# Optimization experiments

Measured on AMD Instinct MI355X. Metric: run time of the kernel, lower is better.

The kernel has to match this reference:

```python
import jax, jax.numpy as jnp
import numpy as np

NUM_ENTS = 100000
NUM_RELS2 = 1000  # num_rels * 2
H_DIM = 128
NUM_EDGES = 2000000
RRELU_SLOPE = (1.0 / 8.0 + 1.0 / 3.0) / 2.0  # F.rrelu eval-mode negative slope


def l2_normalize(x, eps=1e-12):
    # F.normalize along last dim
    n = jnp.sqrt(jnp.sum(x * x, axis=-1, keepdims=True))
    return x / jnp.maximum(n, eps)


def setup_inputs() -> dict:
    key = jax.random.key(0)
    ks = jax.random.split(key, 11)
    s = 1.0 / np.sqrt(H_DIM)
    return {
        "ent_emb": jax.random.normal(ks[0], (NUM_ENTS, H_DIM), jnp.float32),
        "rel_emb": jax.random.normal(ks[1], (NUM_RELS2, H_DIM), jnp.float32) * s,
        "his": jax.random.normal(ks[2], (NUM_ENTS, H_DIM), jnp.float32),
        "W_neighbor": jax.random.normal(ks[3], (H_DIM, H_DIM), jnp.float32) * s,
        "W_self": jax.random.normal(ks[4], (H_DIM, H_DIM), jnp.float32) * s,
        "time_gate_weight": jax.random.normal(ks[5], (H_DIM, H_DIM), jnp.float32) * s,
        "time_gate_bias": jnp.zeros((H_DIM,), jnp.float32),
        "edge_norm": jax.random.uniform(ks[6], (NUM_EDGES,), jnp.float32),
        "src": jax.random.randint(ks[7], (NUM_EDGES,), 0, NUM_ENTS, jnp.int32),
        "dst": jax.random.randint(ks[8], (NUM_EDGES,), 0, NUM_ENTS, jnp.int32),
        "etype": jax.random.randint(ks[9], (NUM_EDGES,), 0, NUM_RELS2, jnp.int32),
    }


def reference(ent_emb, rel_emb, his, W_neighbor, W_self, time_gate_weight,
              time_gate_bias, edge_norm, src, dst, etype):
    # layer_norm=True branch: L2-normalize entity embeddings (F.normalize)
    h = l2_normalize(ent_emb)                                   # [N, D]
    # UnionRGCNLayer message: (h[src] + rel_emb[etype]) @ W, scaled by edge norm
    node = h[src] + rel_emb[etype]                              # [E, D] gather
    msg = (node @ W_neighbor) * edge_norm[:, None]              # [E, D]
    agg = jax.ops.segment_sum(msg, dst, num_segments=NUM_ENTS)  # [N, D] scatter
    # self-loop + rrelu (eval mode: leaky with mean slope)
    h_cur = agg + h @ W_self
    h_cur = jnp.where(h_cur >= 0, h_cur, RRELU_SLOPE * h_cur)
    # time gate: blend current with historical embedding
    gate = jax.nn.sigmoid(h_cur @ time_gate_weight + time_gate_bias)
    out = gate * h_cur + (1.0 - gate) * his
    return out
```

## Files before the change

### kernel.cpp

```cpp
#include <hip/hip_runtime.h>
#include <math.h>

#define NUM_ENTS   100000
#define HD         128
#define NUM_EDGES  2000000
#define NUM_RELS2  1000
#define RRELU_SLOPE 0.22916666666666666f
#define NBLK 391
#define NPAD (NBLK * 256)

#define SB_CNT 391
#define SB_HB  25000
#define SB_RB  125
#define SB_WP  24
#define SB_TOTAL (SB_CNT + SB_HB + SB_RB + SB_WP)

typedef __attribute__((ext_vector_type(8))) short bf16x8;
typedef __attribute__((ext_vector_type(4))) float f32x4;

__device__ __forceinline__ float bf2f(unsigned short h) {
    union { unsigned int u; float f; } v;
    v.u = ((unsigned int)h) << 16;
    return v.f;
}
__device__ __forceinline__ void unpack2(unsigned int u, float& lo, float& hi) {
    union { unsigned int u; float f; } a, b;
    a.u = u << 16;
    b.u = u & 0xffff0000u;
    lo = a.f; hi = b.f;
}
__device__ __forceinline__ unsigned short f2bf(float f) {
    union { float f; unsigned int u; } v; v.f = f;
    unsigned int r = 0x7fffu + ((v.u >> 16) & 1u);
    return (unsigned short)((v.u + r) >> 16);
}

__global__ void __launch_bounds__(256)
setup_kernel(const float* __restrict__ ent, const float* __restrict__ rel,
             const float* __restrict__ Wn, const float* __restrict__ Ws,
             const float* __restrict__ Wt,
             int* __restrict__ cnt, unsigned short* __restrict__ hb,
             unsigned short* __restrict__ rb, unsigned short* __restrict__ Wp) {
    const int bid = blockIdx.x, tid = threadIdx.x;
    if (bid < SB_CNT) {
        cnt[bid * 256 + tid] = 0;
    } else if (bid < SB_CNT + SB_HB) {
        const int row = (bid - SB_CNT) * 4 + (tid >> 6);
        const int lane = tid & 63;
        const float2 v = *(const float2*)(ent + (size_t)row * HD + lane * 2);
        float ss = v.x * v.x + v.y * v.y;
        #pragma unroll
        for (int m = 1; m < 64; m <<= 1) ss += __shfl_xor(ss, m, 64);
        const float inv = 1.0f / fmaxf(sqrtf(ss), 1e-12f);
        const unsigned int o = (unsigned int)f2bf(v.x * inv) |
                               ((unsigned int)f2bf(v.y * inv) << 16);
        *(unsigned int*)(hb + (size_t)row * HD + lane * 2) = o;
    } else if (bid < SB_CNT + SB_HB + SB_RB) {
        const int i = (bid - SB_CNT - SB_HB) * 256 + tid;
        const float4 v = ((const float4*)rel)[i];
        ushort4 o;
        o.x = f2bf(v.x); o.y = f2bf(v.y); o.z = f2bf(v.z); o.w = f2bf(v.w);
        ((ushort4*)rb)[i] = o;
    } else {
        const int blk = (bid - SB_CNT - SB_HB - SB_RB) * 4 + (tid >> 6);
        const int lane = tid & 63;
        const int w = blk >> 5, rem = blk & 31, t = rem >> 2, kt = rem & 3;
        const float* W = (w == 0) ? Wn : (w == 1) ? Ws : Wt;
        const int n  = t * 16 + (lane & 15);
        const int k0 = kt * 32 + (lane >> 4) * 8;
        unsigned short tmp[8];
        #pragma unroll
        for (int j = 0; j < 8; ++j) tmp[j] = f2bf(W[(size_t)(k0 + j) * HD + n]);
        unsigned short* d = Wp + ((size_t)blk * 64 + lane) * 8;
        *(ushort4*)(d + 0) = make_ushort4(tmp[0], tmp[1], tmp[2], tmp[3]);
        *(ushort4*)(d + 4) = make_ushort4(tmp[4], tmp[5], tmp[6], tmp[7]);
    }
}

__global__ void __launch_bounds__(256)
hist_kernel(const int* __restrict__ dst, int* __restrict__ cnt, int* __restrict__ pos) {
    for (int e = blockIdx.x * 256 + threadIdx.x; e < NUM_EDGES; e += gridDim.x * 256)
        pos[e] = atomicAdd(&cnt[dst[e]], 1);
}

__global__ void __launch_bounds__(256)
scan1_kernel(const int* __restrict__ cnt, int* __restrict__ offs, int* __restrict__ bsum) {
    __shared__ int tmp[256];
    const int t = threadIdx.x;
    const int i = blockIdx.x * 256 + t;
    const int v = cnt[i];
    tmp[t] = v;
    __syncthreads();
    #pragma unroll
    for (int d = 1; d < 256; d <<= 1) {
        const int a = (t >= d) ? tmp[t - d] : 0;
        __syncthreads();
        tmp[t] += a;
        __syncthreads();
    }
    offs[i] = tmp[t] - v;
    if (t == 255) bsum[blockIdx.x] = tmp[255];
}

__global__ void __launch_bounds__(512)
scan2_kernel(int* __restrict__ bsum) {
    __shared__ int tmp[512];
    const int t = threadIdx.x;
    const int v = (t < NBLK) ? bsum[t] : 0;
    tmp[t] = v;
    __syncthreads();
    #pragma unroll
    for (int d = 1; d < 512; d <<= 1) {
        const int a = (t >= d) ? tmp[t - d] : 0;
        __syncthreads();
        tmp[t] += a;
        __syncthreads();
    }
    if (t < NBLK) bsum[t] = tmp[t] - v;
}

__global__ void __launch_bounds__(256)
scan3_kernel(int* __restrict__ offs, const int* __restrict__ bsum) {
    const int i = blockIdx.x * 256 + threadIdx.x;
    offs[i] += bsum[blockIdx.x];
}

__global__ void __launch_bounds__(256)
permute_kernel(const int* __restrict__ dst, const int* __restrict__ src,
               const int* __restrict__ ety, const float* __restrict__ enorm,
               const int* __restrict__ offs, const int* __restrict__ pos,
               uint2* __restrict__ recs) {
    for (int e = blockIdx.x * 256 + threadIdx.x; e < NUM_EDGES; e += gridDim.x * 256) {
        const int p = offs[dst[e]] + pos[e];
        uint2 rc;
        rc.x = (unsigned int)src[e] | ((unsigned int)ety[e] << 17);
        rc.y = __float_as_uint(enorm[e]);
        recs[p] = rc;
    }
}

__device__ __forceinline__ void accum8(float* acc, uint4 hv, uint4 rv, float w) {
    float h0, h1, r0, r1;
    unpack2(hv.x, h0, h1); unpack2(rv.x, r0, r1);
    acc[0] += (h0 + r0) * w; acc[1] += (h1 + r1) * w;
    unpack2(hv.y, h0, h1); unpack2(rv.y, r0, r1);
    acc[2] += (h0 + r0) * w; acc[3] += (h1 + r1) * w;
    unpack2(hv.z, h0, h1); unpack2(rv.z, r0, r1);
    acc[4] += (h0 + r0) * w; acc[5] += (h1 + r1) * w;
    unpack2(hv.w, h0, h1); unpack2(rv.w, r0, r1);
    acc[6] += (h0 + r0) * w; acc[7] += (h1 + r1) * w;
}

__global__ void __launch_bounds__(256)
gather_kernel(const unsigned short* __restrict__ hb,
              const unsigned short* __restrict__ rb,
              const int* __restrict__ offs,
              const uint2* __restrict__ recs,
              float* __restrict__ S) {
    const int tid = threadIdx.x;
    const int wv = tid >> 6, lane = tid & 63;
    const int grp = lane >> 4, sub = lane & 15;
    const int d = (blockIdx.x * 4 + wv) * 4 + grp;
    const int beg = offs[d], end = offs[d + 1];
    int i = beg;
    float acc[8] = {0.f, 0.f, 0.f, 0.f, 0.f, 0.f, 0.f, 0.f};
    const unsigned short* hbp = hb + sub * 8;
    const unsigned short* rbp = rb + sub * 8;

    while (__any(i < end)) {
        const bool a0 = i < end, a1 = (i + 1) < end;
        const int j0 = min(i, NUM_EDGES - 1);
        const int j1 = min(i + 1, NUM_EDGES - 1);
        const uint2 rc0 = recs[j0];
        const uint2 rc1 = recs[j1];
        const float w0 = a0 ? __uint_as_float(rc0.y) : 0.f;
        const float w1 = a1 ? __uint_as_float(rc1.y) : 0.f;
        const uint4 hv0 = *(const uint4*)(hbp + (size_t)(rc0.x & 0x1FFFFu) * HD);
        const uint4 rv0 = *(const uint4*)(rbp + (size_t)(rc0.x >> 17) * HD);
        const uint4 hv1 = *(const uint4*)(hbp + (size_t)(rc1.x & 0x1FFFFu) * HD);
        const uint4 rv1 = *(const uint4*)(rbp + (size_t)(rc1.x >> 17) * HD);
        accum8(acc, hv0, rv0, w0);
        accum8(acc, hv1, rv1, w1);
        i += 2;
    }
    float* o = S + (size_t)d * HD + sub * 8;
    *(float4*)(o + 0) = make_float4(acc[0], acc[1], acc[2], acc[3]);
    *(float4*)(o + 4) = make_float4(acc[4], acc[5], acc[6], acc[7]);
}

__global__ void __launch_bounds__(256)
fused_mfma(float* io,
           const unsigned short* __restrict__ hb,
           const unsigned short* __restrict__ Wp,
           const float* __restrict__ bias,
           const float* __restrict__ his) {
    __shared__ unsigned short tile[4][16 * 136];
    const int tid = threadIdx.x;
    const int wv = tid >> 6, lane = tid & 63;
    const int m0 = blockIdx.x * 64 + wv * 16;
    if (m0 >= NUM_ENTS) return;
    const int rA = lane & 15, quad = lane >> 4;
    unsigned short* T = tile[wv];

    #pragma unroll
    for (int i = 0; i < 8; ++i) {
        const int idx = i * 64 + lane;
        const int r = idx >> 5, c4 = idx & 31;
        const float4 v = ((const float4*)(io + (size_t)(m0 + r) * HD))[c4];
        ushort4 o;
        o.x = f2bf(v.x); o.y = f2bf(v.y); o.z = f2bf(v.z); o.w = f2bf(v.w);
        *(ushort4*)(T + r * 136 + c4 * 4) = o;
    }

    const bf16x8* WF = (const bf16x8*)Wp;
    f32x4 acc[8];
    #pragma unroll
    for (int t = 0; t < 8; ++t) acc[t] = (f32x4)0.f;

    #pragma unroll
    for (int ph = 0; ph < 2; ++ph) {
        bf16x8 a[4];
        if (ph == 0) {
            #pragma unroll
            for (int kt = 0; kt < 4; ++kt)
                a[kt] = *(const bf16x8*)(T + rA * 136 + kt * 32 + quad * 8);
        } else {
            const unsigned short* base = hb + (size_t)(m0 + rA) * HD + quad * 8;
            #pragma unroll
            for (int kt = 0; kt < 4; ++kt)
                a[kt] = *(const bf16x8*)(base + kt * 32);
        }
        #pragma unroll
        for (int t = 0; t < 8; ++t) {
            #pragma unroll
            for (int kt = 0; kt < 4; ++kt) {
                const bf16x8 b = WF[(size_t)(ph * 32 + t * 4 + kt) * 64 + lane];
                acc[t] = __builtin_amdgcn_mfma_f32_16x16x32_bf16(a[kt], b, acc[t], 0, 0, 0);
            }
        }
    }

    #pragma unroll
    for (int t = 0; t < 8; ++t)
        #pragma unroll
        for (int r = 0; r < 4; ++r)
            acc[t][r] = acc[t][r] >= 0.f ? acc[t][r] : RRELU_SLOPE * acc[t][r];

    #pragma unroll
    for (int t = 0; t < 8; ++t)
        #pragma unroll
        for (int r = 0; r < 4; ++r)
            T[(quad * 4 + r) * 136 + t * 16 + rA] = f2bf(acc[t][r]);

    bf16x8 a3[4];
    #pragma unroll
    for (int kt = 0; kt < 4; ++kt)
        a3[kt] = *(const bf16x8*)(T + rA * 136 + kt * 32 + quad * 8);

    f32x4 acc2[8];
    #pragma unroll
    for (int t = 0; t < 8; ++t) {
        const float bn = bias[t * 16 + rA];
        acc2[t] = (f32x4){bn, bn, bn, bn};
    }
    #pragma unroll
    for (int t = 0; t < 8; ++t) {
        #pragma unroll
        for (int kt = 0; kt < 4; ++kt) {
            const bf16x8 b = WF[(size_t)(64 + t * 4 + kt) * 64 + lane];
            acc2[t] = __builtin_amdgcn_mfma_f32_16x16x32_bf16(a3[kt], b, acc2[t], 0, 0, 0);
        }
    }

    #pragma unroll
    for (int t = 0; t < 8; ++t) {
        const int col = t * 16 + rA;
        #pragma unroll
        for (int r = 0; r < 4; ++r) {
            const size_t row = (size_t)(m0 + quad * 4 + r);
            const float g = 1.f / (1.f + __expf(-acc2[t][r]));
            const float h = his[row * HD + col];
            io[row * HD + col] = g * acc[t][r] + (1.f - g) * h;
        }
    }
}

extern "C" void kernel_launch(void* const* d_in, const int* in_sizes, int n_in,
                              void* d_out, int out_size, void* d_ws, size_t ws_size,
                              hipStream_t stream) {
    const float* ent   = (const float*)d_in[0];
    const float* rel   = (const float*)d_in[1];
    const float* his   = (const float*)d_in[2];
    const float* Wn    = (const float*)d_in[3];
    const float* Ws    = (const float*)d_in[4];
    const float* Wt    = (const float*)d_in[5];
    const float* bias  = (const float*)d_in[6];
    const float* enorm = (const float*)d_in[7];
    const int* src = (const int*)d_in[8];
    const int* dst = (const int*)d_in[9];
    const int* ety = (const int*)d_in[10];
    float* out = (float*)d_out;

    char* p = (char*)d_ws;
    unsigned short* hb = (unsigned short*)p;  p += (size_t)NUM_ENTS * HD * 2;
    unsigned short* rb = (unsigned short*)p;  p += (size_t)NUM_RELS2 * HD * 2;
    unsigned short* Wp = (unsigned short*)p;  p += (size_t)96 * 64 * 8 * 2;
    int* cnt  = (int*)p;                      p += (size_t)NPAD * 4;
    int* offs = (int*)p;                      p += (size_t)NPAD * 4;
    int* bsum = (int*)p;                      p += 512 * 4;
    int* pos  = (int*)p;                      p += (size_t)NUM_EDGES * 4;
    uint2* recs = (uint2*)p;

    setup_kernel<<<SB_TOTAL, 256, 0, stream>>>(ent, rel, Wn, Ws, Wt, cnt, hb, rb, Wp);
    hist_kernel<<<2048, 256, 0, stream>>>(dst, cnt, pos);
    scan1_kernel<<<NBLK, 256, 0, stream>>>(cnt, offs, bsum);
    scan2_kernel<<<1, 512, 0, stream>>>(bsum);
    scan3_kernel<<<NBLK, 256, 0, stream>>>(offs, bsum);
    permute_kernel<<<2048, 256, 0, stream>>>(dst, src, ety, enorm, offs, pos, recs);
    gather_kernel<<<6250, 256, 0, stream>>>(hb, rb, offs, recs, out );
    fused_mfma<<<(NUM_ENTS + 63) / 64, 256, 0, stream>>>(out, hb, Wp, bias, his);
}
```

Measured before the change: 449.1 us.

## Fuse gather into MFMA kernel and drop per-edge position buffer in CSR build

Merges the per-destination gather and the fused MFMA epilogue into one kernel, so aggregated rows go straight into shared-memory bf16 tiles instead of taking a float round-trip through global memory. The CSR build now takes slots with a second atomic cursor pass instead of storing per-edge positions, removing the pos array traffic. Edge kernels read dst, src, type and norm four at a time with vector loads, and the gather loop software-pipelines its record loads four edges deep. Edge order inside each segment is no longer deterministic, and the fused kernel has fewer blocks to hide gather latency.

```diff
diff --git a/kernel.cpp b/kernel.cpp
--- a/kernel.cpp
+++ b/kernel.cpp
@@ -8,6 +8,8 @@
 #define RRELU_SLOPE 0.22916666666666666f
 #define NBLK 391
 #define NPAD (NBLK * 256)
+#define EQ4  (NUM_EDGES / 4)
+#define EBLK ((EQ4 + 255) / 256)
 
 #define SB_CNT 391
 #define SB_HB  25000
@@ -78,9 +80,15 @@
 }
 
 __global__ void __launch_bounds__(256)
-hist_kernel(const int* __restrict__ dst, int* __restrict__ cnt, int* __restrict__ pos) {
-    for (int e = blockIdx.x * 256 + threadIdx.x; e < NUM_EDGES; e += gridDim.x * 256)
-        pos[e] = atomicAdd(&cnt[dst[e]], 1);
+hist_kernel(const int* __restrict__ dst, int* __restrict__ cnt) {
+    const int i = blockIdx.x * 256 + threadIdx.x;
+    if (i < EQ4) {
+        const int4 d4 = ((const int4*)dst)[i];
+        atomicAdd(&cnt[d4.x], 1);
+        atomicAdd(&cnt[d4.y], 1);
+        atomicAdd(&cnt[d4.z], 1);
+        atomicAdd(&cnt[d4.w], 1);
+    }
 }
 
 __global__ void __launch_bounds__(256)
@@ -120,22 +128,31 @@
 }
 
 __global__ void __launch_bounds__(256)
-scan3_kernel(int* __restrict__ offs, const int* __restrict__ bsum) {
+scan3_kernel(int* __restrict__ offs, const int* __restrict__ bsum, int* __restrict__ cur) {
     const int i = blockIdx.x * 256 + threadIdx.x;
-    offs[i] += bsum[blockIdx.x];
+    const int v = offs[i] + bsum[blockIdx.x];
+    offs[i] = v;
+    cur[i] = v;
 }
 
 __global__ void __launch_bounds__(256)
 permute_kernel(const int* __restrict__ dst, const int* __restrict__ src,
                const int* __restrict__ ety, const float* __restrict__ enorm,
-               const int* __restrict__ offs, const int* __restrict__ pos,
-               uint2* __restrict__ recs) {
-    for (int e = blockIdx.x * 256 + threadIdx.x; e < NUM_EDGES; e += gridDim.x * 256) {
-        const int p = offs[dst[e]] + pos[e];
-        uint2 rc;
-        rc.x = (unsigned int)src[e] | ((unsigned int)ety[e] << 17);
-        rc.y = __float_as_uint(enorm[e]);
-        recs[p] = rc;
+               int* __restrict__ cur, uint2* __restrict__ recs) {
+    const int i = blockIdx.x * 256 + threadIdx.x;
+    if (i < EQ4) {
+        const int4 d4 = ((const int4*)dst)[i];
+        const int4 s4 = ((const int4*)src)[i];
+        const int4 t4 = ((const int4*)ety)[i];
+        const float4 n4 = ((const float4*)enorm)[i];
+        const int p0 = atomicAdd(&cur[d4.x], 1);
+        const int p1 = atomicAdd(&cur[d4.y], 1);
+        const int p2 = atomicAdd(&cur[d4.z], 1);
+        const int p3 = atomicAdd(&cur[d4.w], 1);
+        recs[p0] = make_uint2((unsigned int)s4.x | ((unsigned int)t4.x << 17), __float_as_uint(n4.x));
+        recs[p1] = make_uint2((unsigned int)s4.y | ((unsigned int)t4.y << 17), __float_as_uint(n4.y));
+        recs[p2] = make_uint2((unsigned int)s4.z | ((unsigned int)t4.z << 17), __float_as_uint(n4.z));
+        recs[p3] = make_uint2((unsigned int)s4.w | ((unsigned int)t4.w << 17), __float_as_uint(n4.w));
     }
 }
 
@@ -151,71 +168,62 @@
     acc[6] += (h0 + r0) * w; acc[7] += (h1 + r1) * w;
 }
 
-__global__ void __launch_bounds__(256)
-gather_kernel(const unsigned short* __restrict__ hb,
-              const unsigned short* __restrict__ rb,
-              const int* __restrict__ offs,
-              const uint2* __restrict__ recs,
-              float* __restrict__ S) {
-    const int tid = threadIdx.x;
-    const int wv = tid >> 6, lane = tid & 63;
-    const int grp = lane >> 4, sub = lane & 15;
-    const int d = (blockIdx.x * 4 + wv) * 4 + grp;
-    const int beg = offs[d], end = offs[d + 1];
-    int i = beg;
-    float acc[8] = {0.f, 0.f, 0.f, 0.f, 0.f, 0.f, 0.f, 0.f};
-    const unsigned short* hbp = hb + sub * 8;
-    const unsigned short* rbp = rb + sub * 8;
-
-    while (__any(i < end)) {
-        const bool a0 = i < end, a1 = (i + 1) < end;
-        const int j0 = min(i, NUM_EDGES - 1);
-        const int j1 = min(i + 1, NUM_EDGES - 1);
-        const uint2 rc0 = recs[j0];
-        const uint2 rc1 = recs[j1];
-        const float w0 = a0 ? __uint_as_float(rc0.y) : 0.f;
-        const float w1 = a1 ? __uint_as_float(rc1.y) : 0.f;
-        const uint4 hv0 = *(const uint4*)(hbp + (size_t)(rc0.x & 0x1FFFFu) * HD);
-        const uint4 rv0 = *(const uint4*)(rbp + (size_t)(rc0.x >> 17) * HD);
-        const uint4 hv1 = *(const uint4*)(hbp + (size_t)(rc1.x & 0x1FFFFu) * HD);
-        const uint4 rv1 = *(const uint4*)(rbp + (size_t)(rc1.x >> 17) * HD);
-        accum8(acc, hv0, rv0, w0);
-        accum8(acc, hv1, rv1, w1);
-        i += 2;
-    }
-    float* o = S + (size_t)d * HD + sub * 8;
-    *(float4*)(o + 0) = make_float4(acc[0], acc[1], acc[2], acc[3]);
-    *(float4*)(o + 4) = make_float4(acc[4], acc[5], acc[6], acc[7]);
-}
-
-__global__ void __launch_bounds__(256)
-fused_mfma(float* io,
-           const unsigned short* __restrict__ hb,
-           const unsigned short* __restrict__ Wp,
-           const float* __restrict__ bias,
-           const float* __restrict__ his) {
+__global__ void __launch_bounds__(256, 4)
+gather_mfma(const unsigned short* __restrict__ hb,
+            const unsigned short* __restrict__ rb,
+            const int* __restrict__ offs,
+            const uint2* __restrict__ recs,
+            const unsigned short* __restrict__ Wp,
+            const float* __restrict__ bias,
+            const float* __restrict__ his,
+            float* __restrict__ out) {
     __shared__ unsigned short tile[4][16 * 136];
     const int tid = threadIdx.x;
     const int wv = tid >> 6, lane = tid & 63;
     const int m0 = blockIdx.x * 64 + wv * 16;
     if (m0 >= NUM_ENTS) return;
+    const int grp = lane >> 4, sub = lane & 15;
     const int rA = lane & 15, quad = lane >> 4;
     unsigned short* T = tile[wv];
-
-    #pragma unroll
-    for (int i = 0; i < 8; ++i) {
-        const int idx = i * 64 + lane;
-        const int r = idx >> 5, c4 = idx & 31;
-        const float4 v = ((const float4*)(io + (size_t)(m0 + r) * HD))[c4];
-        ushort4 o;
-        o.x = f2bf(v.x); o.y = f2bf(v.y); o.z = f2bf(v.z); o.w = f2bf(v.w);
-        *(ushort4*)(T + r * 136 + c4 * 4) = o;
+    const unsigned short* hbp = hb + sub * 8;
+    const unsigned short* rbp = rb + sub * 8;
+
+    #pragma unroll
+    for (int b = 0; b < 4; ++b) {
+        const int rloc = b * 4 + grp;
+        const int d = m0 + rloc;
+        const int beg = offs[d], end = offs[d + 1];
+        float acc[8] = {0.f, 0.f, 0.f, 0.f, 0.f, 0.f, 0.f, 0.f};
+        int i = beg;
+        uint2 rcA[4];
+        #pragma unroll
+        for (int k = 0; k < 4; ++k) rcA[k] = recs[min(i + k, NUM_EDGES - 1)];
+        while (__any(i < end)) {
+            uint2 rcB[4];
+            #pragma unroll
+            for (int k = 0; k < 4; ++k) rcB[k] = recs[min(i + 4 + k, NUM_EDGES - 1)];
+            uint4 hv[4], rv[4]; float w[4];
+            #pragma unroll
+            for (int k = 0; k < 4; ++k) {
+                w[k] = (i + k) < end ? __uint_as_float(rcA[k].y) : 0.f;
+                hv[k] = *(const uint4*)(hbp + (size_t)(rcA[k].x & 0x1FFFFu) * HD);
+                rv[k] = *(const uint4*)(rbp + (size_t)(rcA[k].x >> 17) * HD);
+            }
+            #pragma unroll
+            for (int k = 0; k < 4; ++k) accum8(acc, hv[k], rv[k], w[k]);
+            #pragma unroll
+            for (int k = 0; k < 4; ++k) rcA[k] = rcB[k];
+            i += 4;
+        }
+        unsigned short* dT = T + rloc * 136 + sub * 8;
+        *(ushort4*)(dT + 0) = make_ushort4(f2bf(acc[0]), f2bf(acc[1]), f2bf(acc[2]), f2bf(acc[3]));
+        *(ushort4*)(dT + 4) = make_ushort4(f2bf(acc[4]), f2bf(acc[5]), f2bf(acc[6]), f2bf(acc[7]));
     }
 
     const bf16x8* WF = (const bf16x8*)Wp;
-    f32x4 acc[8];
-    #pragma unroll
-    for (int t = 0; t < 8; ++t) acc[t] = (f32x4)0.f;
+    f32x4 acc1[8];
+    #pragma unroll
+    for (int t = 0; t < 8; ++t) acc1[t] = (f32x4)0.f;
 
     #pragma unroll
     for (int ph = 0; ph < 2; ++ph) {
@@ -234,8 +242,8 @@
         for (int t = 0; t < 8; ++t) {
             #pragma unroll
             for (int kt = 0; kt < 4; ++kt) {
-                const bf16x8 b = WF[(size_t)(ph * 32 + t * 4 + kt) * 64 + lane];
-                acc[t] = __builtin_amdgcn_mfma_f32_16x16x32_bf16(a[kt], b, acc[t], 0, 0, 0);
+                const bf16x8 bfr = WF[(size_t)(ph * 32 + t * 4 + kt) * 64 + lane];
+                acc1[t] = __builtin_amdgcn_mfma_f32_16x16x32_bf16(a[kt], bfr, acc1[t], 0, 0, 0);
             }
         }
     }
@@ -244,43 +252,35 @@
     for (int t = 0; t < 8; ++t)
         #pragma unroll
         for (int r = 0; r < 4; ++r)
-            acc[t][r] = acc[t][r] >= 0.f ? acc[t][r] : RRELU_SLOPE * acc[t][r];
+            acc1[t][r] = acc1[t][r] >= 0.f ? acc1[t][r] : RRELU_SLOPE * acc1[t][r];
 
     #pragma unroll
     for (int t = 0; t < 8; ++t)
         #pragma unroll
         for (int r = 0; r < 4; ++r)
-            T[(quad * 4 + r) * 136 + t * 16 + rA] = f2bf(acc[t][r]);
+            T[(quad * 4 + r) * 136 + t * 16 + rA] = f2bf(acc1[t][r]);
 
     bf16x8 a3[4];
     #pragma unroll
     for (int kt = 0; kt < 4; ++kt)
         a3[kt] = *(const bf16x8*)(T + rA * 136 + kt * 32 + quad * 8);
 
-    f32x4 acc2[8];
     #pragma unroll
     for (int t = 0; t < 8; ++t) {
         const float bn = bias[t * 16 + rA];
-        acc2[t] = (f32x4){bn, bn, bn, bn};
-    }
-    #pragma unroll
-    for (int t = 0; t < 8; ++t) {
+        f32x4 c2 = (f32x4){bn, bn, bn, bn};
         #pragma unroll
         for (int kt = 0; kt < 4; ++kt) {
-            const bf16x8 b = WF[(size_t)(64 + t * 4 + kt) * 64 + lane];
-            acc2[t] = __builtin_amdgcn_mfma_f32_16x16x32_bf16(a3[kt], b, acc2[t], 0, 0, 0);
-        }
-    }
-
-    #pragma unroll
-    for (int t = 0; t < 8; ++t) {
+            const bf16x8 bfr = WF[(size_t)(64 + t * 4 + kt) * 64 + lane];
+            c2 = __builtin_amdgcn_mfma_f32_16x16x32_bf16(a3[kt], bfr, c2, 0, 0, 0);
+        }
         const int col = t * 16 + rA;
         #pragma unroll
         for (int r = 0; r < 4; ++r) {
             const size_t row = (size_t)(m0 + quad * 4 + r);
-            const float g = 1.f / (1.f + __expf(-acc2[t][r]));
+            const float g = 1.f / (1.f + __expf(-c2[r]));
             const float h = his[row * HD + col];
-            io[row * HD + col] = g * acc[t][r] + (1.f - g) * h;
+            out[row * HD + col] = g * acc1[t][r] + (1.f - g) * h;
         }
     }
 }
@@ -308,15 +308,13 @@
     int* cnt  = (int*)p;                      p += (size_t)NPAD * 4;
     int* offs = (int*)p;                      p += (size_t)NPAD * 4;
     int* bsum = (int*)p;                      p += 512 * 4;
-    int* pos  = (int*)p;                      p += (size_t)NUM_EDGES * 4;
     uint2* recs = (uint2*)p;
 
     setup_kernel<<<SB_TOTAL, 256, 0, stream>>>(ent, rel, Wn, Ws, Wt, cnt, hb, rb, Wp);
-    hist_kernel<<<2048, 256, 0, stream>>>(dst, cnt, pos);
+    hist_kernel<<<EBLK, 256, 0, stream>>>(dst, cnt);
     scan1_kernel<<<NBLK, 256, 0, stream>>>(cnt, offs, bsum);
     scan2_kernel<<<1, 512, 0, stream>>>(bsum);
-    scan3_kernel<<<NBLK, 256, 0, stream>>>(offs, bsum);
-    permute_kernel<<<2048, 256, 0, stream>>>(dst, src, ety, enorm, offs, pos, recs);
-    gather_kernel<<<6250, 256, 0, stream>>>(hb, rb, offs, recs, out );
-    fused_mfma<<<(NUM_ENTS + 63) / 64, 256, 0, stream>>>(out, hb, Wp, bias, his);
-}
+    scan3_kernel<<<NBLK, 256, 0, stream>>>(offs, bsum, cnt);
+    permute_kernel<<<EBLK, 256, 0, stream>>>(dst, src, ety, enorm, cnt, recs);
+    gather_mfma<<<(NUM_ENTS + 63) / 64, 256, 0, stream>>>(hb, rb, offs, recs, Wp, bias, his, out);
+}
```

After: 530.8 us. 18.2% more time.
